# Performance work log

Measured on AMD Instinct MI355X. Metric: run time of the kernel, lower is better.

Reference implementation:

```python
import jax, jax.numpy as jnp
import numpy as np

N, D, H, B_GRAPHS = 200000, 512, 64, 512


def setup_inputs() -> dict:
    key = jax.random.key(0)
    k1, k2, k3, k4, k5, k6 = jax.random.split(key, 6)
    x = jax.random.normal(k1, (N, D), dtype=jnp.float32)
    batch = jnp.sort(jax.random.randint(k2, (N,), 0, B_GRAPHS, dtype=jnp.int64))
    # attn MLP params: Linear(D,64) -> Tanh -> Linear(64,1)
    s1 = 1.0 / np.sqrt(D)
    s2 = 1.0 / np.sqrt(H)
    W1 = jax.random.uniform(k3, (D, H), jnp.float32, -s1, s1)
    b1 = jax.random.uniform(k4, (H,), jnp.float32, -s1, s1)
    W2 = jax.random.uniform(k5, (H, 1), jnp.float32, -s2, s2)
    b2 = jax.random.uniform(k6, (1,), jnp.float32, -s2, s2)
    return {"x": x, "W1": W1, "b1": b1, "W2": W2, "b2": b2, "batch": batch, "B": B_GRAPHS}


def reference(x, W1, b1, W2, b2, batch, B):
    # scorer MLP: (N,D) -> (N,1)
    scores = jnp.tanh(x @ W1 + b1) @ W2 + b2  # (N,1)
    s = scores[:, 0]  # (N,)
    # segment softmax over nodes grouped by graph id (pyg_softmax semantics)
    seg_max = jax.ops.segment_max(s, batch, num_segments=B)  # (B,)
    seg_max = jnp.where(jnp.isfinite(seg_max), seg_max, 0.0)  # guard empty segments
    e = jnp.exp(s - seg_max[batch])  # (N,)
    denom = jax.ops.segment_sum(e, batch, num_segments=B)  # (B,)
    w = e / (denom[batch] + 1e-16)  # (N,) attention weights
    # weighted scatter-add of node embeddings -> graph embeddings
    out = jax.ops.segment_sum(x * w[:, None], batch, num_segments=B)  # (B,D)
    return out
```

## Files before the change

kernel.cpp:

```cpp
#include <hip/hip_runtime.h>
#include <hip/hip_bf16.h>
#include <math.h>

#define TD 512
#define TH 64
#define CHUNK 16
#define NT 256

typedef __attribute__((ext_vector_type(8))) short bf16x8;
typedef __attribute__((ext_vector_type(4))) float f32x4;

__device__ __forceinline__ unsigned short f2b(float f) {
    return __builtin_bit_cast(unsigned short, __float2bfloat16(f));
}

__device__ __forceinline__ float tanh_fast(float v) {
    float e = __expf(2.0f * v);
    return 1.0f - 2.0f / (e + 1.0f);
}

__device__ __forceinline__ void barrier_lgkm() {
    asm volatile("s_waitcnt lgkmcnt(0)" ::: "memory");
    __builtin_amdgcn_s_barrier();
}

template <int CTRL>
__device__ __forceinline__ float dpp_add(float v) {
    int r = __builtin_amdgcn_update_dpp(0, __builtin_bit_cast(int, v), CTRL, 0xf, 0xf, false);
    return v + __builtin_bit_cast(float, r);
}
__device__ __forceinline__ float row16_sum(float v) {
    v = dpp_add<0x121>(v);
    v = dpp_add<0x122>(v);
    v = dpp_add<0x124>(v);
    v = dpp_add<0x128>(v);
    return v;
}

__global__ void prep_kernel(const int* __restrict__ batch32,
                            const float* __restrict__ W1,
                            int* __restrict__ off,
                            unsigned short* __restrict__ W1B,
                            int N, int B) {
    int i = blockIdx.x * blockDim.x + threadIdx.x;
    if (i < TH * TD) {
        int c = i >> 9;
        int k = i & 511;
        W1B[i] = f2b(W1[k * TH + c]);
    }
    if (i >= N) return;
    const bool is64 = (batch32[N - 1] == 0);
    auto bval = [&](int kk) -> int { return is64 ? batch32[2 * kk] : batch32[kk]; };
    int bc = bval(i);
    if (i == 0) {
        for (int j = 0; j <= bc; ++j) off[j] = 0;
    } else {
        int bp = bval(i - 1);
        for (int j = bp + 1; j <= bc; ++j) off[j] = i;
    }
    if (i == N - 1) {
        for (int j = bc + 1; j <= B; ++j) off[j] = N;
    }
}

__global__ __launch_bounds__(NT)
__attribute__((amdgpu_waves_per_eu(2, 2)))
void attnpool_kernel(const float* __restrict__ x,
                     const unsigned short* __restrict__ W1B,
                     const float* __restrict__ b1,
                     const float* __restrict__ W2,
                     const float* __restrict__ b2,
                     const int* __restrict__ off,
                     float* __restrict__ out,
                     int N)
{
    __shared__ __align__(16) char smem[TH * TD * 2];
    __shared__ float sP[4][CHUNK];
    __shared__ float lsum;
    unsigned short* W1T   = (unsigned short*)smem;
    unsigned short* Atile = (unsigned short*)smem;

    const int tid  = threadIdx.x;
    const int b    = blockIdx.x;
    const int lane = tid & 63;
    const int ct   = tid >> 6;

    const int seg_start = off[b];
    const int seg_len   = off[b + 1] - seg_start;
    const float b2v = b2[0];

    const int rowcls = tid >> 7;
    const int col4   = (tid & 127) << 2;

    const int jcol = (ct << 4) + (lane & 15);
    const int kb   = (lane >> 4) << 3;
    const float b1v = b1[jcol];
    const float w2v = W2[jcol];

    float4 accw; accw.x = 0.f; accw.y = 0.f; accw.z = 0.f; accw.w = 0.f;
    float l_part = 0.0f;
    float4 xrA[8], xrB[8];

    auto load_chunk = [&](float4 (&xr)[8], int c0) {
        #pragma unroll
        for (int p = 0; p < 8; ++p) {
            int rl = (p << 1) + rowcls;
            int r  = c0 + rl;
            int gr = (r < seg_len) ? (seg_start + r) : seg_start;
            xr[p] = *reinterpret_cast<const float4*>(&x[(size_t)gr * TD + col4]);
        }
    };

    if (seg_len > 0) load_chunk(xrA, 0);

    {
        const bf16x8* W1B8 = reinterpret_cast<const bf16x8*>(W1B);
        #pragma unroll
        for (int i = 0; i < (TH * TD / 8) / NT; ++i) {
            int e8 = tid + NT * i;
            int c  = e8 >> 6;
            int k8 = e8 & 63;
            bf16x8 v = W1B8[e8];
            *reinterpret_cast<bf16x8*>(&W1T[(c * TD + (k8 << 3)) ^ ((c & 7) << 3)]) = v;
        }
    }
    barrier_lgkm();

    bf16x8 w1f[16];
    #pragma unroll
    for (int kk = 0; kk < 16; ++kk) {
        w1f[kk] = *reinterpret_cast<const bf16x8*>(
            &W1T[(jcol * TD + (kk << 5) + kb) ^ ((jcol & 7) << 3)]);
    }
    barrier_lgkm();

    auto body = [&](float4 (&cur)[8], float4 (&nxt)[8], int c0) {
        if (c0 + CHUNK < seg_len) load_chunk(nxt, c0 + CHUNK);

        #pragma unroll
        for (int p = 0; p < 8; ++p) {
            int rl = (p << 1) + rowcls;
            ushort4 v;
            v.x = f2b(cur[p].x); v.y = f2b(cur[p].y);
            v.z = f2b(cur[p].z); v.w = f2b(cur[p].w);
            *reinterpret_cast<ushort4*>(&Atile[(rl * TD + col4) ^ ((rl & 7) << 3)]) = v;
        }
        barrier_lgkm();

        f32x4 acc = {0, 0, 0, 0};
        const int rA = lane & 15;
        #pragma unroll
        for (int kk = 0; kk < 16; ++kk) {
            int k0 = (kk << 5) + kb;
            bf16x8 av = *reinterpret_cast<const bf16x8*>(
                &Atile[(rA * TD + k0) ^ ((rA & 7) << 3)]);
            acc = __builtin_amdgcn_mfma_f32_16x16x32_bf16(av, w1f[kk], acc, 0, 0, 0);
        }

        {
            float pv[4];
            #pragma unroll
            for (int q = 0; q < 4; ++q)
                pv[q] = row16_sum(tanh_fast(acc[q] + b1v) * w2v);
            if ((lane & 15) == 0) {
                int g = lane >> 4;
                #pragma unroll
                for (int q = 0; q < 4; ++q)
                    sP[ct][(g << 2) + q] = pv[q];
            }
        }
        barrier_lgkm();

        float ev;
        {
            int r = lane & 15;
            float s = sP[0][r] + sP[1][r] + sP[2][r] + sP[3][r] + b2v;
            ev = ((c0 + r) < seg_len) ? __expf(s) : 0.0f;
            if (ct == 0 && lane < CHUNK) l_part += ev;
        }

        #pragma unroll
        for (int p = 0; p < 8; ++p) {
            float wgt = __shfl(ev, (p << 1) + rowcls, 64);
            accw.x += wgt * cur[p].x;
            accw.y += wgt * cur[p].y;
            accw.z += wgt * cur[p].z;
            accw.w += wgt * cur[p].w;
        }
    };

    if (seg_len > 0) {
        int c0 = 0;
        while (true) {
            body(xrA, xrB, c0);
            c0 += CHUNK;
            if (c0 >= seg_len) break;
            body(xrB, xrA, c0);
            c0 += CHUNK;
            if (c0 >= seg_len) break;
        }
    }

    float* fs = reinterpret_cast<float*>(Atile);
    __syncthreads();
    *reinterpret_cast<float4*>(&fs[rowcls * TD + col4]) = accw;
    if (ct == 0) {
        float ls = l_part;
        #pragma unroll
        for (int m = 1; m < 64; m <<= 1) ls += __shfl_xor(ls, m, 64);
        if (lane == 0) lsum = ls;
    }
    __syncthreads();
    float inv = 1.0f / (lsum + 1e-16f);
    out[(size_t)b * TD + tid]       = (fs[tid] + fs[TD + tid]) * inv;
    out[(size_t)b * TD + 256 + tid] = (fs[256 + tid] + fs[TD + 256 + tid]) * inv;
}

extern "C" void kernel_launch(void* const* d_in, const int* in_sizes, int n_in,
                              void* d_out, int out_size, void* d_ws, size_t ws_size,
                              hipStream_t stream) {
    const float* x  = (const float*)d_in[0];
    const float* W1 = (const float*)d_in[1];
    const float* b1 = (const float*)d_in[2];
    const float* W2 = (const float*)d_in[3];
    const float* b2 = (const float*)d_in[4];
    const int* batch = (const int*)d_in[5];
    int N = in_sizes[5];
    int B = out_size / TD;
    if (B <= 0 || N <= 0) return;

    int* off = (int*)d_ws;
    unsigned short* W1B = (unsigned short*)((char*)d_ws + 4096);

    int prep_elems = (N > TH * TD) ? N : TH * TD;
    prep_kernel<<<dim3((prep_elems + 255) / 256), dim3(256), 0, stream>>>(
        batch, W1, off, W1B, N, B);
    attnpool_kernel<<<dim3(B), dim3(NT), 0, stream>>>(
        x, W1B, b1, W2, b2, off, (float*)d_out, N);
}
```

Baseline: 87.28 us.

## Double block size to 512 threads with split-K MFMA and deeper prefetch

```diff
diff --git a/kernel.cpp b/kernel.cpp
--- a/kernel.cpp
+++ b/kernel.cpp
@@ -5,7 +5,7 @@
 #define TD 512
 #define TH 64
 #define CHUNK 16
-#define NT 256
+#define NT 512
 
 typedef __attribute__((ext_vector_type(8))) short bf16x8;
 typedef __attribute__((ext_vector_type(4))) float f32x4;
@@ -63,8 +63,7 @@
     }
 }
 
-__global__ __launch_bounds__(NT)
-__attribute__((amdgpu_waves_per_eu(2, 2)))
+__global__ __launch_bounds__(NT, 4)
 void attnpool_kernel(const float* __restrict__ x,
                      const unsigned short* __restrict__ W1B,
                      const float* __restrict__ b1,
@@ -75,15 +74,21 @@
                      int N)
 {
     __shared__ __align__(16) char smem[TH * TD * 2];
-    __shared__ float sP[4][CHUNK];
+    __shared__ float b1s[TH];
+    __shared__ float W2s[TH];
+    __shared__ float sE[CHUNK];
     __shared__ float lsum;
     unsigned short* W1T   = (unsigned short*)smem;
     unsigned short* Atile = (unsigned short*)smem;
+    float*          sPre  = (float*)(smem + CHUNK * TD * 2);
 
     const int tid  = threadIdx.x;
     const int b    = blockIdx.x;
     const int lane = tid & 63;
-    const int ct   = tid >> 6;
+    const int w    = tid >> 6;
+    const int ct   = w & 3;
+    const int kh   = w >> 2;
+    const int kh256 = kh << 8;
 
     const int seg_start = off[b];
     const int seg_len   = off[b + 1] - seg_start;
@@ -94,24 +99,22 @@
 
     const int jcol = (ct << 4) + (lane & 15);
     const int kb   = (lane >> 4) << 3;
-    const float b1v = b1[jcol];
-    const float w2v = W2[jcol];
 
     float4 accw; accw.x = 0.f; accw.y = 0.f; accw.z = 0.f; accw.w = 0.f;
     float l_part = 0.0f;
-    float4 xrA[8], xrB[8];
-
-    auto load_chunk = [&](float4 (&xr)[8], int c0) {
-        #pragma unroll
-        for (int p = 0; p < 8; ++p) {
-            int rl = (p << 1) + rowcls;
+    float4 xrA[4], xrB[4], xrC[4];
+
+    auto load_chunk = [&](float4 (&xr)[4], int c0) {
+        #pragma unroll
+        for (int p = 0; p < 4; ++p) {
+            int rl = (p << 2) + rowcls;
             int r  = c0 + rl;
             int gr = (r < seg_len) ? (seg_start + r) : seg_start;
             xr[p] = *reinterpret_cast<const float4*>(&x[(size_t)gr * TD + col4]);
         }
     };
 
-    if (seg_len > 0) load_chunk(xrA, 0);
+    if (seg_len > 0) { load_chunk(xrA, 0); load_chunk(xrB, CHUNK); }
 
     {
         const bf16x8* W1B8 = reinterpret_cast<const bf16x8*>(W1B);
@@ -124,22 +127,23 @@
             *reinterpret_cast<bf16x8*>(&W1T[(c * TD + (k8 << 3)) ^ ((c & 7) << 3)]) = v;
         }
     }
+    if (tid < TH) { b1s[tid] = b1[tid]; W2s[tid] = W2[tid]; }
     barrier_lgkm();
 
-    bf16x8 w1f[16];
+    bf16x8 w1f[8];
     #pragma unroll
-    for (int kk = 0; kk < 16; ++kk) {
+    for (int kk = 0; kk < 8; ++kk) {
         w1f[kk] = *reinterpret_cast<const bf16x8*>(
-            &W1T[(jcol * TD + (kk << 5) + kb) ^ ((jcol & 7) << 3)]);
+            &W1T[(jcol * TD + kh256 + (kk << 5) + kb) ^ ((jcol & 7) << 3)]);
     }
     barrier_lgkm();
 
-    auto body = [&](float4 (&cur)[8], float4 (&nxt)[8], int c0) {
-        if (c0 + CHUNK < seg_len) load_chunk(nxt, c0 + CHUNK);
-
-        #pragma unroll
-        for (int p = 0; p < 8; ++p) {
-            int rl = (p << 1) + rowcls;
+    auto body = [&](float4 (&cur)[4], float4 (&pre)[4], int c0) {
+        if (c0 + 2 * CHUNK < seg_len) load_chunk(pre, c0 + 2 * CHUNK);
+
+        #pragma unroll
+        for (int p = 0; p < 4; ++p) {
+            int rl = (p << 2) + rowcls;
             ushort4 v;
             v.x = f2b(cur[p].x); v.y = f2b(cur[p].y);
             v.z = f2b(cur[p].z); v.w = f2b(cur[p].w);
@@ -150,61 +154,65 @@
         f32x4 acc = {0, 0, 0, 0};
         const int rA = lane & 15;
         #pragma unroll
-        for (int kk = 0; kk < 16; ++kk) {
-            int k0 = (kk << 5) + kb;
+        for (int kk = 0; kk < 8; ++kk) {
+            int k0 = kh256 + (kk << 5) + kb;
             bf16x8 av = *reinterpret_cast<const bf16x8*>(
                 &Atile[(rA * TD + k0) ^ ((rA & 7) << 3)]);
             acc = __builtin_amdgcn_mfma_f32_16x16x32_bf16(av, w1f[kk], acc, 0, 0, 0);
         }
-
         {
-            float pv[4];
+            int g = lane >> 4;
             #pragma unroll
-            for (int q = 0; q < 4; ++q)
-                pv[q] = row16_sum(tanh_fast(acc[q] + b1v) * w2v);
-            if ((lane & 15) == 0) {
-                int g = lane >> 4;
-                #pragma unroll
-                for (int q = 0; q < 4; ++q)
-                    sP[ct][(g << 2) + q] = pv[q];
+            for (int q = 0; q < 4; ++q) {
+                int r = (g << 2) + q;
+                sPre[(kh << 10) + (r << 6) + jcol] = acc[q];
             }
         }
         barrier_lgkm();
 
-        float ev;
-        {
-            int r = lane & 15;
-            float s = sP[0][r] + sP[1][r] + sP[2][r] + sP[3][r] + b2v;
-            ev = ((c0 + r) < seg_len) ? __expf(s) : 0.0f;
-            if (ct == 0 && lane < CHUNK) l_part += ev;
-        }
-
-        #pragma unroll
-        for (int p = 0; p < 8; ++p) {
-            float wgt = __shfl(ev, (p << 1) + rowcls, 64);
+        #pragma unroll
+        for (int h = 0; h < 2; ++h) {
+            int rr = w + (h << 3);
+            float pv = sPre[(rr << 6) + lane] + sPre[1024 + (rr << 6) + lane];
+            float sv = tanh_fast(pv + b1s[lane]) * W2s[lane];
+            sv = row16_sum(sv);
+            sv += __shfl_xor(sv, 16, 64);
+            sv += __shfl_xor(sv, 32, 64);
+            if (lane == 0)
+                sE[rr] = ((c0 + rr) < seg_len) ? __expf(sv + b2v) : 0.0f;
+        }
+        barrier_lgkm();
+
+        #pragma unroll
+        for (int p = 0; p < 4; ++p) {
+            float wgt = sE[(p << 2) + rowcls];
             accw.x += wgt * cur[p].x;
             accw.y += wgt * cur[p].y;
             accw.z += wgt * cur[p].z;
             accw.w += wgt * cur[p].w;
         }
+        if (w == 0 && lane < CHUNK) l_part += sE[lane];
     };
 
     if (seg_len > 0) {
         int c0 = 0;
         while (true) {
-            body(xrA, xrB, c0);
+            body(xrA, xrC, c0);
             c0 += CHUNK;
             if (c0 >= seg_len) break;
             body(xrB, xrA, c0);
             c0 += CHUNK;
             if (c0 >= seg_len) break;
-        }
-    }
-
-    float* fs = reinterpret_cast<float*>(Atile);
+            body(xrC, xrB, c0);
+            c0 += CHUNK;
+            if (c0 >= seg_len) break;
+        }
+    }
+
+    float* fs = reinterpret_cast<float*>(smem);
     __syncthreads();
     *reinterpret_cast<float4*>(&fs[rowcls * TD + col4]) = accw;
-    if (ct == 0) {
+    if (w == 0) {
         float ls = l_part;
         #pragma unroll
         for (int m = 1; m < 64; m <<= 1) ls += __shfl_xor(ls, m, 64);
@@ -212,8 +220,8 @@
     }
     __syncthreads();
     float inv = 1.0f / (lsum + 1e-16f);
-    out[(size_t)b * TD + tid]       = (fs[tid] + fs[TD + tid]) * inv;
-    out[(size_t)b * TD + 256 + tid] = (fs[256 + tid] + fs[TD + 256 + tid]) * inv;
+    out[(size_t)b * TD + tid] =
+        (fs[tid] + fs[TD + tid] + fs[2 * TD + tid] + fs[3 * TD + tid]) * inv;
 }
 
 extern "C" void kernel_launch(void* const* d_in, const int* in_sizes, int n_in,
```

Result: slower. 90.26 us (+3.4%).

## Split each segment across two blocks with atomic accumulation and a normalize pass

Applied to the files above, without the earlier changes.

```diff
diff --git a/kernel.cpp b/kernel.cpp
--- a/kernel.cpp
+++ b/kernel.cpp
@@ -41,8 +41,12 @@
                             const float* __restrict__ W1,
                             int* __restrict__ off,
                             unsigned short* __restrict__ W1B,
+                            float* __restrict__ outp,
+                            float* __restrict__ denom,
                             int N, int B) {
     int i = blockIdx.x * blockDim.x + threadIdx.x;
+    if (i < B * TD) outp[i] = 0.0f;
+    if (i < B) denom[i] = 0.0f;
     if (i < TH * TD) {
         int c = i >> 9;
         int k = i & 511;
@@ -63,30 +67,37 @@
     }
 }
 
-__global__ __launch_bounds__(NT)
-__attribute__((amdgpu_waves_per_eu(2, 2)))
+__global__ void norm_kernel(float* __restrict__ outp,
+                            const float* __restrict__ denom, int total) {
+    int i = blockIdx.x * blockDim.x + threadIdx.x;
+    if (i < total) outp[i] = outp[i] / (denom[i >> 9] + 1e-16f);
+}
+
+__global__ __launch_bounds__(NT, 4)
 void attnpool_kernel(const float* __restrict__ x,
                      const unsigned short* __restrict__ W1B,
                      const float* __restrict__ b1,
                      const float* __restrict__ W2,
                      const float* __restrict__ b2,
                      const int* __restrict__ off,
-                     float* __restrict__ out,
+                     float* __restrict__ outp,
+                     float* __restrict__ denom,
                      int N)
 {
-    __shared__ __align__(16) char smem[TH * TD * 2];
+    __shared__ __align__(16) unsigned short Atile[CHUNK * TD];
     __shared__ float sP[4][CHUNK];
-    __shared__ float lsum;
-    unsigned short* W1T   = (unsigned short*)smem;
-    unsigned short* Atile = (unsigned short*)smem;
 
     const int tid  = threadIdx.x;
-    const int b    = blockIdx.x;
+    const int b    = blockIdx.x >> 1;
+    const int half = blockIdx.x & 1;
     const int lane = tid & 63;
     const int ct   = tid >> 6;
 
-    const int seg_start = off[b];
-    const int seg_len   = off[b + 1] - seg_start;
+    const int s0   = off[b];
+    const int lful = off[b + 1] - s0;
+    const int h0   = (lful + 1) >> 1;
+    const int seg_start = half ? (s0 + h0) : s0;
+    const int seg_len   = half ? (lful - h0) : h0;
     const float b2v = b2[0];
 
     const int rowcls = tid >> 7;
@@ -113,26 +124,11 @@
 
     if (seg_len > 0) load_chunk(xrA, 0);
 
-    {
-        const bf16x8* W1B8 = reinterpret_cast<const bf16x8*>(W1B);
-        #pragma unroll
-        for (int i = 0; i < (TH * TD / 8) / NT; ++i) {
-            int e8 = tid + NT * i;
-            int c  = e8 >> 6;
-            int k8 = e8 & 63;
-            bf16x8 v = W1B8[e8];
-            *reinterpret_cast<bf16x8*>(&W1T[(c * TD + (k8 << 3)) ^ ((c & 7) << 3)]) = v;
-        }
-    }
-    barrier_lgkm();
-
     bf16x8 w1f[16];
     #pragma unroll
     for (int kk = 0; kk < 16; ++kk) {
-        w1f[kk] = *reinterpret_cast<const bf16x8*>(
-            &W1T[(jcol * TD + (kk << 5) + kb) ^ ((jcol & 7) << 3)]);
-    }
-    barrier_lgkm();
+        w1f[kk] = *reinterpret_cast<const bf16x8*>(&W1B[jcol * TD + (kk << 5) + kb]);
+    }
 
     auto body = [&](float4 (&cur)[8], float4 (&nxt)[8], int c0) {
         if (c0 + CHUNK < seg_len) load_chunk(nxt, c0 + CHUNK);
@@ -199,21 +195,16 @@
             c0 += CHUNK;
             if (c0 >= seg_len) break;
         }
-    }
-
-    float* fs = reinterpret_cast<float*>(Atile);
-    __syncthreads();
-    *reinterpret_cast<float4*>(&fs[rowcls * TD + col4]) = accw;
-    if (ct == 0) {
-        float ls = l_part;
-        #pragma unroll
-        for (int m = 1; m < 64; m <<= 1) ls += __shfl_xor(ls, m, 64);
-        if (lane == 0) lsum = ls;
-    }
-    __syncthreads();
-    float inv = 1.0f / (lsum + 1e-16f);
-    out[(size_t)b * TD + tid]       = (fs[tid] + fs[TD + tid]) * inv;
-    out[(size_t)b * TD + 256 + tid] = (fs[256 + tid] + fs[TD + 256 + tid]) * inv;
+
+        atomicAdd(&outp[(size_t)b * TD + col4 + 0], accw.x);
+        atomicAdd(&outp[(size_t)b * TD + col4 + 1], accw.y);
+        atomicAdd(&outp[(size_t)b * TD + col4 + 2], accw.z);
+        atomicAdd(&outp[(size_t)b * TD + col4 + 3], accw.w);
+        if (ct == 0) {
+            float ls = row16_sum(l_part);
+            if (lane == 0) atomicAdd(&denom[b], ls);
+        }
+    }
 }
 
 extern "C" void kernel_launch(void* const* d_in, const int* in_sizes, int n_in,
@@ -231,10 +222,16 @@
 
     int* off = (int*)d_ws;
     unsigned short* W1B = (unsigned short*)((char*)d_ws + 4096);
-
-    int prep_elems = (N > TH * TD) ? N : TH * TD;
+    float* denom = (float*)((char*)d_ws + 4096 + TH * TD * 2);
+    float* outp  = (float*)d_out;
+
+    int prep_elems = N;
+    if (B * TD > prep_elems) prep_elems = B * TD;
+    if (TH * TD > prep_elems) prep_elems = TH * TD;
     prep_kernel<<<dim3((prep_elems + 255) / 256), dim3(256), 0, stream>>>(
-        batch, W1, off, W1B, N, B);
-    attnpool_kernel<<<dim3(B), dim3(NT), 0, stream>>>(
-        x, W1B, b1, W2, b2, off, (float*)d_out, N);
-}
+        batch, W1, off, W1B, outp, denom, N, B);
+    attnpool_kernel<<<dim3(2 * B), dim3(NT), 0, stream>>>(
+        x, W1B, b1, W2, b2, off, outp, denom, N);
+    norm_kernel<<<dim3((B * TD + 255) / 256), dim3(256), 0, stream>>>(
+        outp, denom, B * TD);
+}
```

Result: slower. 309.2 us (+254.3%).
